# Kernel optimization log

Hardware: AMD Instinct MI355X
Metric: run time of the kernel (lower is better)

Reference implementation:

```python
import jax, jax.numpy as jnp
import numpy as np

N_NODES = 100000
N_EDGES = 1600000
N_CLASS = 26
HIDDEN = 128
K = 3  # TAGConv hops


def setup_inputs() -> dict:
    key = jax.random.key(0)
    ks = jax.random.split(key, 12)
    x = jax.random.normal(ks[0], (N_NODES, N_CLASS), dtype=jnp.float32)
    edge_index = jax.random.randint(ks[1], (2, N_EDGES), 0, N_NODES, dtype=jnp.int64)
    edge_weight = jax.random.uniform(ks[2], (N_EDGES,), dtype=jnp.float32)
    # Per-hop weights (K+1 hops incl. hop 0) for each of the 3 TAGConv layers.
    def lin(k, fan_in, fan_out):
        s = 1.0 / np.sqrt(fan_in)
        return jax.random.uniform(k, (K + 1, fan_in, fan_out), dtype=jnp.float32, minval=-s, maxval=s)
    W1 = lin(ks[3], N_CLASS, HIDDEN)
    b1 = jnp.zeros((HIDDEN,), dtype=jnp.float32)
    W2 = lin(ks[4], HIDDEN, HIDDEN)
    b2 = jnp.zeros((HIDDEN,), dtype=jnp.float32)
    W3 = lin(ks[5], HIDDEN, N_CLASS)
    b3 = jnp.zeros((N_CLASS,), dtype=jnp.float32)
    return {"x": x, "edge_index": edge_index, "edge_weight": edge_weight,
            "W1": W1, "b1": b1, "W2": W2, "b2": b2, "W3": W3, "b3": b3}


def _gcn_norm(edge_index, edge_weight, n):
    # symmetric normalization deg^-1/2 * w * deg^-1/2, no self loops (PyG TAGConv)
    row, col = edge_index[0], edge_index[1]
    deg = jax.ops.segment_sum(edge_weight, col, num_segments=n)
    dinv = jnp.where(deg > 0, jax.lax.rsqrt(jnp.maximum(deg, 1e-12)), 0.0)
    return dinv[row] * edge_weight * dinv[col]


def _tag_conv(x, row, col, norm, W, b, n):
    # out = sum_k W_k(x_k), x_0 = x, x_k = A_norm x_{k-1}
    out = x @ W[0]
    h = x
    for k in range(1, K + 1):
        h = jax.ops.segment_sum(norm[:, None] * h[row], col, num_segments=n)
        out = out + h @ W[k]
    return out + b


def reference(x, edge_index, edge_weight, W1, b1, W2, b2, W3, b3):
    n = x.shape[0]
    row, col = edge_index[0], edge_index[1]
    norm = _gcn_norm(edge_index, edge_weight, n)  # identical for all 3 layers
    h = jax.nn.elu(_tag_conv(x, row, col, norm, W1, b1, n))
    h = jax.nn.elu(_tag_conv(h, row, col, norm, W2, b2, n))
    return _tag_conv(h, row, col, norm, W3, b3, n)
```

## Files before the change

kernel.cpp:

```cpp
#include <hip/hip_runtime.h>

#define NCLS 26
#define HID 128
#define EPB 8192
#define MAXBK 512
#define BCAP 6016
typedef unsigned short ushort_t;
typedef unsigned int uint_t;
typedef unsigned long long u64;

typedef __bf16 bf16x8 __attribute__((ext_vector_type(8)));
typedef float f32x4 __attribute__((ext_vector_type(4)));
typedef unsigned int u32x4 __attribute__((ext_vector_type(4)));
typedef unsigned int u32x2 __attribute__((ext_vector_type(2)));

static __device__ __forceinline__ float b2f(ushort_t h) {
  return __uint_as_float(((uint_t)h) << 16);
}
static __device__ __forceinline__ ushort_t f2b(float f) {
  uint_t u = __float_as_uint(f);
  uint_t r = (u + 0x7fffu + ((u >> 16) & 1u)) >> 16;
  return (ushort_t)r;
}
static __device__ __forceinline__ uint_t pack2(float f0, float f1) {
  return (uint_t)f2b(f0) | ((uint_t)f2b(f1) << 16);
}
static __device__ __forceinline__ float lo16(uint_t v) { return b2f((ushort_t)(v & 0xffffu)); }
static __device__ __forceinline__ float hi16(uint_t v) { return b2f((ushort_t)(v >> 16)); }
static __device__ __forceinline__ bf16x8 ld_frag(const ushort_t* p) {
  u32x4 v = *reinterpret_cast<const u32x4*>(p);
  return __builtin_bit_cast(bf16x8, v);
}


__global__ __launch_bounds__(256) void bucket_place(
    const int* __restrict__ ei, const float* __restrict__ ew,
    int* __restrict__ gcur, u64* __restrict__ bkt, int E, int nbk) {
  __shared__ uint_t lc[MAXBK];
  __shared__ uint_t lb[MAXBK];
  int tid = threadIdx.x;
  for (int t = tid; t < nbk; t += 256) lc[t] = 0;
  __syncthreads();
  int e0 = blockIdx.x * EPB;
#pragma unroll
  for (int i = 0; i < EPB / 256; ++i) {
    int e = e0 + tid + i * 256;
    if (e < E) atomicAdd(&lc[(uint_t)ei[E + e] >> 8], 1u);
  }
  __syncthreads();
  for (int t = tid; t < nbk; t += 256) {
    uint_t c = lc[t];
    lb[t] = c ? (uint_t)t * BCAP + (uint_t)atomicAdd(&gcur[t], (int)c) : 0u;
    lc[t] = 0;
  }
  __syncthreads();
#pragma unroll
  for (int i = 0; i < EPB / 256; ++i) {
    int e = e0 + tid + i * 256;
    if (e < E) {
      uint_t r = (uint_t)ei[e];
      uint_t c = (uint_t)ei[E + e];
      uint_t b = c >> 8;
      uint_t pos = lb[b] + atomicAdd(&lc[b], 1u);
      bkt[pos] = ((u64)(r | ((c & 255u) << 24)) << 32) | (u64)__float_as_uint(ew[e]);
    }
  }
}

__global__ void scan_buckets(const int* __restrict__ gcur, int* __restrict__ mbase,
                             int nbk, int E) {
  __shared__ int s[512];
  int t = threadIdx.x;
  int v = (t < nbk) ? gcur[t] : 0;
  s[t] = v;
  __syncthreads();
  for (int off = 1; off < 512; off <<= 1) {
    int u = (t >= off) ? s[t - off] : 0;
    __syncthreads();
    s[t] += u;
    __syncthreads();
  }
  if (t < nbk) mbase[t] = s[t] - v;
  if (t == 0) mbase[nbk] = E;
}

__global__ __launch_bounds__(256) void bucket_stats(
    const u64* __restrict__ bkt, const int* __restrict__ gcur, const int* __restrict__ mbase,
    int* __restrict__ start, float* __restrict__ dinv, int n, int E) {
  int b = blockIdx.x;
  __shared__ uint_t cnt[256];
  __shared__ float deg[256];
  __shared__ int ssc[256];
  int tid = threadIdx.x;
  cnt[tid] = 0;
  deg[tid] = 0.f;
  __syncthreads();
  int fill = gcur[b];
  const u64* w = bkt + (size_t)b * BCAP;
  for (int p = tid; p < fill; p += 256) {
    u64 v = w[p];
    uint_t cl = (uint_t)(v >> 56);
    float wv = __uint_as_float((uint_t)(v & 0xffffffffULL));
    atomicAdd(&cnt[cl], 1u);
    atomicAdd(&deg[cl], wv);
  }
  __syncthreads();
  int v0 = (int)cnt[tid];
  ssc[tid] = v0;
  __syncthreads();
  for (int off = 1; off < 256; off <<= 1) {
    int u = (tid >= off) ? ssc[tid - off] : 0;
    __syncthreads();
    ssc[tid] += u;
    __syncthreads();
  }
  int node = (b << 8) + tid;
  if (node < n) {
    start[node] = mbase[b] + ssc[tid] - v0;
    float d = deg[tid];
    dinv[node] = d > 0.f ? rsqrtf(fmaxf(d, 1e-12f)) : 0.f;
  }
  if (b == 0 && tid == 0) start[n] = E;
}

__global__ __launch_bounds__(256) void bucket_emit(
    const u64* __restrict__ bkt, const int* __restrict__ gcur, const int* __restrict__ start,
    const float* __restrict__ dinv, u32x2* __restrict__ meta, int n) {
  int b = blockIdx.x;
  __shared__ uint_t lcur[256];
  int tid = threadIdx.x;
  lcur[tid] = 0;
  __syncthreads();
  int fill = gcur[b];
  const u64* w = bkt + (size_t)b * BCAP;
  for (int p = tid; p < fill; p += 256) {
    u64 v = w[p];
    uint_t hi = (uint_t)(v >> 32);
    uint_t r = hi & 0xffffffu;
    uint_t cl = hi >> 24;
    float wv = __uint_as_float((uint_t)(v & 0xffffffffULL));
    uint_t node = ((uint_t)b << 8) + cl;
    float nrm = dinv[r] * wv * dinv[node];
    uint_t slot = (uint_t)start[node] + atomicAdd(&lcur[cl], 1u);
    u32x2 m;
    m.x = r;
    m.y = __float_as_uint(nrm);
    meta[slot] = m;
  }
}

__global__ __launch_bounds__(256) void prep_misc(
    const float* __restrict__ x, uint_t* __restrict__ x32,
    const float* __restrict__ W1, ushort_t* __restrict__ Wz1,
    const float* __restrict__ W2, ushort_t* __restrict__ Wz2,
    const float* __restrict__ W3, ushort_t* __restrict__ Wz3, int n, int gconv) {
  int blk = blockIdx.x;
  int tid = threadIdx.x;
  if (blk < gconv) {
    int idx = blk * 256 + tid;
    if (idx >= n * 16) return;
    int node = idx >> 4, lane = idx & 15;
    float f0 = 0.f, f1 = 0.f;
    if (lane < 13) {
      f0 = x[node * 26 + 2 * lane];
      f1 = x[node * 26 + 2 * lane + 1];
    }
    x32[idx] = pack2(f0, f1);
  } else if (blk < gconv + 64) {
    int idx = (blk - gconv) * 256 + tid;
    int i = idx & 7, l = (idx >> 3) & 63, j = (idx >> 9) & 7, t = idx >> 12;
    int k = 8 * (l >> 4) + i;
    int col = 16 * j + (l & 15);
    float v = (k < NCLS) ? W1[((size_t)t * NCLS + k) * 128 + col] : 0.f;
    Wz1[idx] = f2b(v);
  } else if (blk < gconv + 64 + 256) {
    int idx = (blk - gconv - 64) * 256 + tid;
    int i = idx & 7, l = (idx >> 3) & 63, j = (idx >> 9) & 7, t = idx >> 12;
    int s = t >> 2, tt = t & 3;
    int k = tt * 32 + 8 * (l >> 4) + i;
    int col = 16 * j + (l & 15);
    float v = W2[((size_t)s * HID + k) * 128 + col];
    Wz2[idx] = f2b(v);
  } else {
    int idx = (blk - gconv - 64 - 256) * 256 + tid;
    int i = idx & 7, l = (idx >> 3) & 63, j = (idx >> 9) & 7, t = idx >> 12;
    int k = t * 32 + 8 * (l >> 4) + i;
    int col = 16 * j + (l & 15);
    int s = col >> 5, c = col & 31;
    float v = (c < 26) ? W3[((size_t)s * 128 + k) * 26 + c] : 0.f;
    Wz3[idx] = f2b(v);
  }
}


__global__ __launch_bounds__(256) void spmm128_bf(
    const u32x2* __restrict__ meta, const int* __restrict__ start,
    const uint_t* __restrict__ in, uint_t* __restrict__ out, int n) {
  int node = blockIdx.x * 4 + (threadIdx.x >> 6);
  int lane = threadIdx.x & 63;
  if (node >= n) return;
  int s = start[node], m = start[node + 1] - s;
  int eq = lane >> 4;
  uint_t foff = (uint_t)(lane & 15) << 4;
  const char* inb = (const char*)in;
  float a0 = 0.f, a1 = 0.f, a2 = 0.f, a3 = 0.f, a4 = 0.f, a5 = 0.f, a6 = 0.f, a7 = 0.f;
  if (m > 0) {
    const int mm = m - 1;
    u32x2 mtA0 = meta[s + (eq < m ? eq : mm)];
    u32x2 mtA1 = meta[s + (4 + eq < m ? 4 + eq : mm)];
    u32x2 mtB0 = meta[s + (8 + eq < m ? 8 + eq : mm)];
    u32x2 mtB1 = meta[s + (12 + eq < m ? 12 + eq : mm)];
    u32x4 vA0 = *reinterpret_cast<const u32x4*>(inb + (((uint_t)mtA0.x << 8) + foff));
    u32x4 vA1 = *reinterpret_cast<const u32x4*>(inb + (((uint_t)mtA1.x << 8) + foff));
    for (int base = 0; base < m; base += 8) {
      int p0 = base + 16 + eq, p1 = base + 20 + eq;
      u32x2 mtC0 = meta[s + (p0 < m ? p0 : mm)];
      u32x2 mtC1 = meta[s + (p1 < m ? p1 : mm)];
      u32x4 vB0 = *reinterpret_cast<const u32x4*>(inb + (((uint_t)mtB0.x << 8) + foff));
      u32x4 vB1 = *reinterpret_cast<const u32x4*>(inb + (((uint_t)mtB1.x << 8) + foff));
      float w0 = (base + eq < m) ? __uint_as_float(mtA0.y) : 0.f;
      float w1 = (base + 4 + eq < m) ? __uint_as_float(mtA1.y) : 0.f;
      a0 += w0 * lo16(vA0.x); a1 += w0 * hi16(vA0.x);
      a2 += w0 * lo16(vA0.y); a3 += w0 * hi16(vA0.y);
      a4 += w0 * lo16(vA0.z); a5 += w0 * hi16(vA0.z);
      a6 += w0 * lo16(vA0.w); a7 += w0 * hi16(vA0.w);
      a0 += w1 * lo16(vA1.x); a1 += w1 * hi16(vA1.x);
      a2 += w1 * lo16(vA1.y); a3 += w1 * hi16(vA1.y);
      a4 += w1 * lo16(vA1.z); a5 += w1 * hi16(vA1.z);
      a6 += w1 * lo16(vA1.w); a7 += w1 * hi16(vA1.w);
      mtA0 = mtB0; mtA1 = mtB1;
      mtB0 = mtC0; mtB1 = mtC1;
      vA0 = vB0; vA1 = vB1;
    }
  }
  a0 += __shfl_xor(a0, 16); a1 += __shfl_xor(a1, 16);
  a2 += __shfl_xor(a2, 16); a3 += __shfl_xor(a3, 16);
  a4 += __shfl_xor(a4, 16); a5 += __shfl_xor(a5, 16);
  a6 += __shfl_xor(a6, 16); a7 += __shfl_xor(a7, 16);
  a0 += __shfl_xor(a0, 32); a1 += __shfl_xor(a1, 32);
  a2 += __shfl_xor(a2, 32); a3 += __shfl_xor(a3, 32);
  a4 += __shfl_xor(a4, 32); a5 += __shfl_xor(a5, 32);
  a6 += __shfl_xor(a6, 32); a7 += __shfl_xor(a7, 32);
  if (eq == 0) {
    u32x4 o;
    o.x = pack2(a0, a1);
    o.y = pack2(a2, a3);
    o.z = pack2(a4, a5);
    o.w = pack2(a6, a7);
    *reinterpret_cast<u32x4*>(out + (size_t)node * 64 + (foff >> 2)) = o;
  }
}

__global__ __launch_bounds__(256) void spmm26_bf(
    const u32x2* __restrict__ meta, const int* __restrict__ start,
    const uint_t* __restrict__ in, const uint_t* __restrict__ add,
    uint_t* __restrict__ out, int n) {
  int node = blockIdx.x * 32 + (threadIdx.x >> 3);
  int ln = threadIdx.x & 7;
  if (node >= n) return;
  int s = start[node], m = start[node + 1] - s;
  uint_t foff = (uint_t)ln << 3;
  const char* inb = (const char*)in;
  float a0 = 0.f, a1 = 0.f, a2 = 0.f, a3 = 0.f;
  if (m > 0) {
    for (int base = 0; base < m; base += 8) {
      int j = base + ln;
      u32x2 mt = meta[s + (j < m ? j : m - 1)];
      int rr = (int)mt.x;
      float ww = (j < m) ? __uint_as_float(mt.y) : 0.f;
#pragma unroll
      for (int k = 0; k < 8; ++k) {
        uint_t r = (uint_t)__shfl(rr, k, 8);
        float wv = __shfl(ww, k, 8);
        u32x2 v = *reinterpret_cast<const u32x2*>(inb + ((r << 6) + foff));
        a0 += wv * lo16(v.x); a1 += wv * hi16(v.x);
        a2 += wv * lo16(v.y); a3 += wv * hi16(v.y);
      }
    }
  }
  if (add) {
    u32x2 v = *reinterpret_cast<const u32x2*>(add + (size_t)node * 16 + 2 * ln);
    a0 += lo16(v.x); a1 += hi16(v.x);
    a2 += lo16(v.y); a3 += hi16(v.y);
  }
  u32x2 o;
  o.x = pack2(a0, a1);
  o.y = pack2(a2, a3);
  *reinterpret_cast<u32x2*>(out + (size_t)node * 16 + 2 * ln) = o;
}

__global__ __launch_bounds__(256) void spmm26_addf(
    const u32x2* __restrict__ meta, const int* __restrict__ start,
    const uint_t* __restrict__ in, float* __restrict__ out, int n) {
  int node = blockIdx.x * 32 + (threadIdx.x >> 3);
  int ln = threadIdx.x & 7;
  if (node >= n) return;
  int s = start[node], m = start[node + 1] - s;
  uint_t foff = (uint_t)ln << 3;
  const char* inb = (const char*)in;
  float a0 = 0.f, a1 = 0.f, a2 = 0.f, a3 = 0.f;
  if (m > 0) {
    for (int base = 0; base < m; base += 8) {
      int j = base + ln;
      u32x2 mt = meta[s + (j < m ? j : m - 1)];
      int rr = (int)mt.x;
      float ww = (j < m) ? __uint_as_float(mt.y) : 0.f;
#pragma unroll
      for (int k = 0; k < 8; ++k) {
        uint_t r = (uint_t)__shfl(rr, k, 8);
        float wv = __shfl(ww, k, 8);
        u32x2 v = *reinterpret_cast<const u32x2*>(inb + ((r << 6) + foff));
        a0 += wv * lo16(v.x); a1 += wv * hi16(v.x);
        a2 += wv * lo16(v.y); a3 += wv * hi16(v.y);
      }
    }
  }
  int c0 = 4 * ln;
  if (c0 + 0 < 26) out[(size_t)node * 26 + c0 + 0] += a0;
  if (c0 + 1 < 26) out[(size_t)node * 26 + c0 + 1] += a1;
  if (c0 + 2 < 26) out[(size_t)node * 26 + c0 + 2] += a2;
  if (c0 + 3 < 26) out[(size_t)node * 26 + c0 + 3] += a3;
}

template <int KW, int NSRC, int EPI, int GROUP>
__global__ __launch_bounds__(256) void mfma_gemm(
    const ushort_t* __restrict__ A0, const ushort_t* __restrict__ A1,
    const ushort_t* __restrict__ A2, const ushort_t* __restrict__ A3,
    const ushort_t* __restrict__ Wswz, const float* __restrict__ bias,
    ushort_t* __restrict__ outb, float* __restrict__ outf, int n) {
  constexpr int KSPS = KW / 32;
  constexpr int KSTEPS = NSRC * KSPS;
  constexpr int NGROUPS = KSTEPS / GROUP;
  __shared__ ushort_t sW[GROUP * 4096];
  const int tid = threadIdx.x;
  const int w = tid >> 6;
  const int l = tid & 63;
  const int row0 = blockIdx.x * 64 + w * 16;
  const int koff = 8 * (l >> 4);
  const int arow = row0 + (l & 15);
  const int arow_c = arow < n ? arow : (n - 1);

  f32x4 acc[8];
#pragma unroll
  for (int j = 0; j < 8; ++j) acc[j] = (f32x4){0.f, 0.f, 0.f, 0.f};

  const ushort_t* const srcs[4] = {A0, A1, A2, A3};

  auto aload = [&](int t) {
    const int s = t / KSPS;
    const int tt = t - s * KSPS;
    return ld_frag(srcs[s] + (size_t)arow_c * KW + tt * 32 + koff);
  };

  bf16x8 afA[GROUP], afB[GROUP];
#pragma unroll
  for (int c = 0; c < GROUP; ++c) afA[c] = aload(c);
  u32x4 gw[2 * GROUP];
#pragma unroll
  for (int c = 0; c < GROUP; ++c) {
    const ushort_t* p = Wswz + (size_t)c * 4096 + tid * 8;
    gw[2 * c] = *reinterpret_cast<const u32x4*>(p);
    gw[2 * c + 1] = *reinterpret_cast<const u32x4*>(p + 2048);
  }

#pragma unroll
  for (int g = 0; g < NGROUPS; ++g) {
    __syncthreads();
#pragma unroll
    for (int c = 0; c < GROUP; ++c) {
      *reinterpret_cast<u32x4*>(sW + c * 4096 + tid * 8) = gw[2 * c];
      *reinterpret_cast<u32x4*>(sW + c * 4096 + tid * 8 + 2048) = gw[2 * c + 1];
    }
    if (g + 1 < NGROUPS) {
#pragma unroll
      for (int c = 0; c < GROUP; ++c) {
        const ushort_t* p = Wswz + (size_t)(g + 1) * GROUP * 4096 + (size_t)c * 4096 + tid * 8;
        gw[2 * c] = *reinterpret_cast<const u32x4*>(p);
        gw[2 * c + 1] = *reinterpret_cast<const u32x4*>(p + 2048);
      }
#pragma unroll
      for (int c = 0; c < GROUP; ++c) {
        if (g & 1)
          afA[c] = aload((g + 1) * GROUP + c);
        else
          afB[c] = aload((g + 1) * GROUP + c);
      }
    }
    __syncthreads();
#pragma unroll
    for (int tg = 0; tg < GROUP; ++tg) {
      bf16x8 af = (g & 1) ? afB[tg] : afA[tg];
      const ushort_t* wp = sW + tg * 4096 + l * 8;
#pragma unroll
      for (int j = 0; j < 8; ++j) {
        bf16x8 bfr = ld_frag(wp + j * 64 * 8);
        acc[j] = __builtin_amdgcn_mfma_f32_16x16x32_bf16(af, bfr, acc[j], 0, 0, 0);
      }
    }
  }

  const int ccol = l & 15;
  const int crow0 = row0 + 4 * (l >> 4);
#pragma unroll
  for (int j = 0; j < 8; ++j) {
    if (EPI == 0) {
      int col = 16 * j + ccol;
      float bi = bias[col];
#pragma unroll
      for (int r = 0; r < 4; ++r) {
        int row = crow0 + r;
        if (row >= n) continue;
        float v = acc[j][r] + bi;
        v = v > 0.f ? v : (__expf(v) - 1.f);
        outb[(size_t)row * 128 + col] = f2b(v);
      }
    } else {
      int slot = j >> 1;
      int c = 16 * (j & 1) + ccol;
#pragma unroll
      for (int r = 0; r < 4; ++r) {
        int row = crow0 + r;
        if (row >= n) continue;
        float v = acc[j][r];
        if (slot == 0) {
          if (c < 26) outf[(size_t)row * 26 + c] = v + bias[c];
        } else {
          outb[((size_t)(slot - 1) * n + row) * 32 + c] = f2b(v);
        }
      }
    }
  }
}


extern "C" void kernel_launch(void* const* d_in, const int* in_sizes, int n_in,
                              void* d_out, int out_size, void* d_ws, size_t ws_size,
                              hipStream_t stream) {
  const float* x  = (const float*)d_in[0];
  const int*   ei = (const int*)d_in[1];
  const float* ew = (const float*)d_in[2];
  const float* W1 = (const float*)d_in[3];
  const float* b1 = (const float*)d_in[4];
  const float* W2 = (const float*)d_in[5];
  const float* b2 = (const float*)d_in[6];
  const float* W3 = (const float*)d_in[7];
  const float* b3 = (const float*)d_in[8];
  float* out = (float*)d_out;

  const int n = in_sizes[0] / NCLS;
  const int E = in_sizes[2];
  const int nbk = (n + 255) >> 8;

  char* w = (char*)d_ws;
  auto alloc = [&](size_t bytes) {
    char* p = w;
    w += (bytes + 255) / 256 * 256;
    return p;
  };
  uint_t* H0 = (uint_t*)alloc((size_t)n * 64 * 4);
  uint_t* P1 = (uint_t*)alloc((size_t)n * 64 * 4);
  uint_t* P2 = (uint_t*)alloc((size_t)n * 64 * 4);
  uint_t* P3 = (uint_t*)alloc((size_t)n * 64 * 4);
  uint_t* H1 = (uint_t*)alloc((size_t)n * 64 * 4);
  uint_t* x32 = (uint_t*)alloc((size_t)n * 16 * 4);
  uint_t* q1  = (uint_t*)alloc((size_t)n * 16 * 4);
  uint_t* q2  = (uint_t*)alloc((size_t)n * 16 * 4);
  uint_t* q3  = (uint_t*)alloc((size_t)n * 16 * 4);
  uint_t* zb  = (uint_t*)alloc((size_t)n * 48 * 4);
  ushort_t* Wz1 = (ushort_t*)alloc(4 * 4096 * 2);
  ushort_t* Wz2 = (ushort_t*)alloc(16 * 4096 * 2);
  ushort_t* Wz3 = (ushort_t*)alloc(4 * 4096 * 2);
  u64*   bkt  = (u64*)zb;
  u32x2* meta = (u32x2*)alloc((size_t)E * 8);
  int*   start = (int*)alloc((size_t)(n + 1) * 4);
  float* dinv  = (float*)alloc((size_t)n * 4);
  int*   gcur  = (int*)alloc(MAXBK * 4);
  int*   mbase = (int*)alloc((MAXBK + 1) * 4);

  const int ab = (E + EPB - 1) / EPB;
  const int gconv = (n * 16 + 255) / 256;

  prep_misc<<<gconv + 64 + 256 + 64, 256, 0, stream>>>(x, x32, W1, Wz1, W2, Wz2, W3, Wz3,
                                                       n, gconv);

  hipMemsetAsync(gcur, 0, MAXBK * 4, stream);
  bucket_place<<<ab, 256, 0, stream>>>(ei, ew, gcur, bkt, E, nbk);
  scan_buckets<<<1, 512, 0, stream>>>(gcur, mbase, nbk, E);
  bucket_stats<<<nbk, 256, 0, stream>>>(bkt, gcur, mbase, start, dinv, n, E);
  bucket_emit<<<nbk, 256, 0, stream>>>(bkt, gcur, start, dinv, meta, n);

  const int g128 = (n + 3) / 4;
  const int g26  = (n + 31) / 32;
  const int gg   = (n + 63) / 64;

  spmm26_bf<<<g26, 256, 0, stream>>>(meta, start, x32, nullptr, q1, n);
  spmm26_bf<<<g26, 256, 0, stream>>>(meta, start, q1, nullptr, q2, n);
  spmm26_bf<<<g26, 256, 0, stream>>>(meta, start, q2, nullptr, q3, n);
  mfma_gemm<32, 4, 0, 4><<<gg, 256, 0, stream>>>(
      (const ushort_t*)x32, (const ushort_t*)q1, (const ushort_t*)q2, (const ushort_t*)q3,
      Wz1, b1, (ushort_t*)H0, nullptr, n);

  spmm128_bf<<<g128, 256, 0, stream>>>(meta, start, H0, P1, n);
  spmm128_bf<<<g128, 256, 0, stream>>>(meta, start, P1, P2, n);
  spmm128_bf<<<g128, 256, 0, stream>>>(meta, start, P2, P3, n);
  mfma_gemm<128, 4, 0, 4><<<gg, 256, 0, stream>>>(
      (const ushort_t*)H0, (const ushort_t*)P1, (const ushort_t*)P2, (const ushort_t*)P3,
      Wz2, b2, (ushort_t*)H1, nullptr, n);

  mfma_gemm<128, 1, 1, 4><<<gg, 256, 0, stream>>>(
      (const ushort_t*)H1, (const ushort_t*)H1, (const ushort_t*)H1, (const ushort_t*)H1,
      Wz3, b3, (ushort_t*)zb, out, n);

  uint_t* z1 = zb;
  uint_t* z2 = zb + (size_t)n * 16;
  uint_t* z3 = zb + (size_t)n * 32;
  spmm26_bf<<<g26, 256, 0, stream>>>(meta, start, z3, z2, q1, n);
  spmm26_bf<<<g26, 256, 0, stream>>>(meta, start, q1, z1, q2, n);
  spmm26_addf<<<g26, 256, 0, stream>>>(meta, start, q2, out, n);
}
```

Baseline: 452.6 us.

## Pad per-node CSR edge lists to multiples of eight with zero entries

Measured after the change: 455.5 us. No clear change (+0.6%).

```diff
diff --git a/kernel.cpp b/kernel.cpp
--- a/kernel.cpp
+++ b/kernel.cpp
@@ -67,26 +67,9 @@
   }
 }
 
-__global__ void scan_buckets(const int* __restrict__ gcur, int* __restrict__ mbase,
-                             int nbk, int E) {
-  __shared__ int s[512];
-  int t = threadIdx.x;
-  int v = (t < nbk) ? gcur[t] : 0;
-  s[t] = v;
-  __syncthreads();
-  for (int off = 1; off < 512; off <<= 1) {
-    int u = (t >= off) ? s[t - off] : 0;
-    __syncthreads();
-    s[t] += u;
-    __syncthreads();
-  }
-  if (t < nbk) mbase[t] = s[t] - v;
-  if (t == 0) mbase[nbk] = E;
-}
-
 __global__ __launch_bounds__(256) void bucket_stats(
-    const u64* __restrict__ bkt, const int* __restrict__ gcur, const int* __restrict__ mbase,
-    int* __restrict__ start, float* __restrict__ dinv, int n, int E) {
+    const u64* __restrict__ bkt, const int* __restrict__ gcur,
+    int* __restrict__ start, int* __restrict__ pbs, float* __restrict__ dinv, int n) {
   int b = blockIdx.x;
   __shared__ uint_t cnt[256];
   __shared__ float deg[256];
@@ -105,8 +88,8 @@
     atomicAdd(&deg[cl], wv);
   }
   __syncthreads();
-  int v0 = (int)cnt[tid];
-  ssc[tid] = v0;
+  int pc = ((int)cnt[tid] + 7) & ~7;
+  ssc[tid] = pc;
   __syncthreads();
   for (int off = 1; off < 256; off <<= 1) {
     int u = (tid >= off) ? ssc[tid - off] : 0;
@@ -116,19 +99,47 @@
   }
   int node = (b << 8) + tid;
   if (node < n) {
-    start[node] = mbase[b] + ssc[tid] - v0;
+    start[node] = ssc[tid] - pc;
     float d = deg[tid];
     dinv[node] = d > 0.f ? rsqrtf(fmaxf(d, 1e-12f)) : 0.f;
   }
-  if (b == 0 && tid == 0) start[n] = E;
+  if (tid == 255) pbs[b] = ssc[255];
+}
+
+__global__ void scan_pb(const int* __restrict__ pbs, int* __restrict__ pbase,
+                        int* __restrict__ start, int nbk, int n) {
+  __shared__ int s[512];
+  int t = threadIdx.x;
+  int v = (t < nbk) ? pbs[t] : 0;
+  s[t] = v;
+  __syncthreads();
+  for (int off = 1; off < 512; off <<= 1) {
+    int u = (t >= off) ? s[t - off] : 0;
+    __syncthreads();
+    s[t] += u;
+    __syncthreads();
+  }
+  if (t < nbk) pbase[t] = s[t] - v;
+  if (t == 0) {
+    pbase[nbk] = s[nbk - 1 < 512 ? nbk - 1 : 511];
+    start[n] = pbase[nbk];
+  }
 }
 
 __global__ __launch_bounds__(256) void bucket_emit(
-    const u64* __restrict__ bkt, const int* __restrict__ gcur, const int* __restrict__ start,
-    const float* __restrict__ dinv, u32x2* __restrict__ meta, int n) {
+    const u64* __restrict__ bkt, const int* __restrict__ gcur, const int* __restrict__ pbase,
+    int* __restrict__ start, const float* __restrict__ dinv, u32x2* __restrict__ meta, int n) {
   int b = blockIdx.x;
   __shared__ uint_t lcur[256];
+  __shared__ int sstart[256];
   int tid = threadIdx.x;
+  int node = (b << 8) + tid;
+  int bb = pbase[b];
+  int fin = 0;
+  if (node < n) {
+    fin = start[node] + bb;
+    sstart[tid] = fin;
+  }
   lcur[tid] = 0;
   __syncthreads();
   int fill = gcur[b];
@@ -139,13 +150,23 @@
     uint_t r = hi & 0xffffffu;
     uint_t cl = hi >> 24;
     float wv = __uint_as_float((uint_t)(v & 0xffffffffULL));
-    uint_t node = ((uint_t)b << 8) + cl;
-    float nrm = dinv[r] * wv * dinv[node];
-    uint_t slot = (uint_t)start[node] + atomicAdd(&lcur[cl], 1u);
+    uint_t nd = ((uint_t)b << 8) + cl;
+    float nrm = dinv[r] * wv * dinv[nd];
+    uint_t slot = (uint_t)sstart[cl] + atomicAdd(&lcur[cl], 1u);
     u32x2 m;
     m.x = r;
     m.y = __float_as_uint(nrm);
     meta[slot] = m;
+  }
+  __syncthreads();
+  if (node < n) {
+    start[node] = fin;
+    int c = (int)lcur[tid];
+    int pc = (c + 7) & ~7;
+    u32x2 z;
+    z.x = 0u;
+    z.y = 0u;
+    for (int i = c; i < pc; ++i) meta[fin + i] = z;
   }
 }
 
@@ -199,27 +220,33 @@
   int node = blockIdx.x * 4 + (threadIdx.x >> 6);
   int lane = threadIdx.x & 63;
   if (node >= n) return;
-  int s = start[node], m = start[node + 1] - s;
+  int s = start[node], mp = start[node + 1] - s;
   int eq = lane >> 4;
   uint_t foff = (uint_t)(lane & 15) << 4;
   const char* inb = (const char*)in;
   float a0 = 0.f, a1 = 0.f, a2 = 0.f, a3 = 0.f, a4 = 0.f, a5 = 0.f, a6 = 0.f, a7 = 0.f;
-  if (m > 0) {
-    const int mm = m - 1;
-    u32x2 mtA0 = meta[s + (eq < m ? eq : mm)];
-    u32x2 mtA1 = meta[s + (4 + eq < m ? 4 + eq : mm)];
-    u32x2 mtB0 = meta[s + (8 + eq < m ? 8 + eq : mm)];
-    u32x2 mtB1 = meta[s + (12 + eq < m ? 12 + eq : mm)];
+  if (mp > 0) {
+    u32x2 mtA0 = meta[s + eq];
+    u32x2 mtA1 = meta[s + 4 + eq];
+    int i8 = 8 + eq;
+    if (i8 >= mp) i8 = mp - 1;
+    int i12 = 12 + eq;
+    if (i12 >= mp) i12 = mp - 1;
+    u32x2 mtB0 = meta[s + i8];
+    u32x2 mtB1 = meta[s + i12];
     u32x4 vA0 = *reinterpret_cast<const u32x4*>(inb + (((uint_t)mtA0.x << 8) + foff));
     u32x4 vA1 = *reinterpret_cast<const u32x4*>(inb + (((uint_t)mtA1.x << 8) + foff));
-    for (int base = 0; base < m; base += 8) {
-      int p0 = base + 16 + eq, p1 = base + 20 + eq;
-      u32x2 mtC0 = meta[s + (p0 < m ? p0 : mm)];
-      u32x2 mtC1 = meta[s + (p1 < m ? p1 : mm)];
+    for (int base = 0; base < mp; base += 8) {
+      int p0 = base + 16 + eq;
+      p0 = p0 < mp ? p0 : mp - 1;
+      int p1 = base + 20 + eq;
+      p1 = p1 < mp ? p1 : mp - 1;
+      u32x2 mtC0 = meta[s + p0];
+      u32x2 mtC1 = meta[s + p1];
       u32x4 vB0 = *reinterpret_cast<const u32x4*>(inb + (((uint_t)mtB0.x << 8) + foff));
       u32x4 vB1 = *reinterpret_cast<const u32x4*>(inb + (((uint_t)mtB1.x << 8) + foff));
-      float w0 = (base + eq < m) ? __uint_as_float(mtA0.y) : 0.f;
-      float w1 = (base + 4 + eq < m) ? __uint_as_float(mtA1.y) : 0.f;
+      float w0 = __uint_as_float(mtA0.y);
+      float w1 = __uint_as_float(mtA1.y);
       a0 += w0 * lo16(vA0.x); a1 += w0 * hi16(vA0.x);
       a2 += w0 * lo16(vA0.y); a3 += w0 * hi16(vA0.y);
       a4 += w0 * lo16(vA0.z); a5 += w0 * hi16(vA0.z);
@@ -258,24 +285,21 @@
   int node = blockIdx.x * 32 + (threadIdx.x >> 3);
   int ln = threadIdx.x & 7;
   if (node >= n) return;
-  int s = start[node], m = start[node + 1] - s;
+  int s = start[node], mp = start[node + 1] - s;
   uint_t foff = (uint_t)ln << 3;
   const char* inb = (const char*)in;
   float a0 = 0.f, a1 = 0.f, a2 = 0.f, a3 = 0.f;
-  if (m > 0) {
-    for (int base = 0; base < m; base += 8) {
-      int j = base + ln;
-      u32x2 mt = meta[s + (j < m ? j : m - 1)];
-      int rr = (int)mt.x;
-      float ww = (j < m) ? __uint_as_float(mt.y) : 0.f;
-#pragma unroll
-      for (int k = 0; k < 8; ++k) {
-        uint_t r = (uint_t)__shfl(rr, k, 8);
-        float wv = __shfl(ww, k, 8);
-        u32x2 v = *reinterpret_cast<const u32x2*>(inb + ((r << 6) + foff));
-        a0 += wv * lo16(v.x); a1 += wv * hi16(v.x);
-        a2 += wv * lo16(v.y); a3 += wv * hi16(v.y);
-      }
+  for (int base = 0; base < mp; base += 8) {
+    u32x2 mt = meta[s + base + ln];
+    int rr = (int)mt.x;
+    float ww = __uint_as_float(mt.y);
+#pragma unroll
+    for (int k = 0; k < 8; ++k) {
+      uint_t r = (uint_t)__shfl(rr, k, 8);
+      float wv = __shfl(ww, k, 8);
+      u32x2 v = *reinterpret_cast<const u32x2*>(inb + ((r << 6) + foff));
+      a0 += wv * lo16(v.x); a1 += wv * hi16(v.x);
+      a2 += wv * lo16(v.y); a3 += wv * hi16(v.y);
     }
   }
   if (add) {
@@ -295,24 +319,21 @@
   int node = blockIdx.x * 32 + (threadIdx.x >> 3);
   int ln = threadIdx.x & 7;
   if (node >= n) return;
-  int s = start[node], m = start[node + 1] - s;
+  int s = start[node], mp = start[node + 1] - s;
   uint_t foff = (uint_t)ln << 3;
   const char* inb = (const char*)in;
   float a0 = 0.f, a1 = 0.f, a2 = 0.f, a3 = 0.f;
-  if (m > 0) {
-    for (int base = 0; base < m; base += 8) {
-      int j = base + ln;
-      u32x2 mt = meta[s + (j < m ? j : m - 1)];
-      int rr = (int)mt.x;
-      float ww = (j < m) ? __uint_as_float(mt.y) : 0.f;
-#pragma unroll
-      for (int k = 0; k < 8; ++k) {
-        uint_t r = (uint_t)__shfl(rr, k, 8);
-        float wv = __shfl(ww, k, 8);
-        u32x2 v = *reinterpret_cast<const u32x2*>(inb + ((r << 6) + foff));
-        a0 += wv * lo16(v.x); a1 += wv * hi16(v.x);
-        a2 += wv * lo16(v.y); a3 += wv * hi16(v.y);
-      }
+  for (int base = 0; base < mp; base += 8) {
+    u32x2 mt = meta[s + base + ln];
+    int rr = (int)mt.x;
+    float ww = __uint_as_float(mt.y);
+#pragma unroll
+    for (int k = 0; k < 8; ++k) {
+      uint_t r = (uint_t)__shfl(rr, k, 8);
+      float wv = __shfl(ww, k, 8);
+      u32x2 v = *reinterpret_cast<const u32x2*>(inb + ((r << 6) + foff));
+      a0 += wv * lo16(v.x); a1 += wv * hi16(v.x);
+      a2 += wv * lo16(v.y); a3 += wv * hi16(v.y);
     }
   }
   int c0 = 4 * ln;
@@ -471,11 +492,12 @@
   ushort_t* Wz2 = (ushort_t*)alloc(16 * 4096 * 2);
   ushort_t* Wz3 = (ushort_t*)alloc(4 * 4096 * 2);
   u64*   bkt  = (u64*)zb;
-  u32x2* meta = (u32x2*)alloc((size_t)E * 8);
+  u32x2* meta = (u32x2*)alloc(((size_t)E + 7 * (size_t)n + 64) * 8);
   int*   start = (int*)alloc((size_t)(n + 1) * 4);
   float* dinv  = (float*)alloc((size_t)n * 4);
   int*   gcur  = (int*)alloc(MAXBK * 4);
-  int*   mbase = (int*)alloc((MAXBK + 1) * 4);
+  int*   pbs   = (int*)alloc(MAXBK * 4);
+  int*   pbase = (int*)alloc((MAXBK + 1) * 4);
 
   const int ab = (E + EPB - 1) / EPB;
   const int gconv = (n * 16 + 255) / 256;
@@ -485,9 +507,9 @@
 
   hipMemsetAsync(gcur, 0, MAXBK * 4, stream);
   bucket_place<<<ab, 256, 0, stream>>>(ei, ew, gcur, bkt, E, nbk);
-  scan_buckets<<<1, 512, 0, stream>>>(gcur, mbase, nbk, E);
-  bucket_stats<<<nbk, 256, 0, stream>>>(bkt, gcur, mbase, start, dinv, n, E);
-  bucket_emit<<<nbk, 256, 0, stream>>>(bkt, gcur, start, dinv, meta, n);
+  bucket_stats<<<nbk, 256, 0, stream>>>(bkt, gcur, start, pbs, dinv, n);
+  scan_pb<<<1, 512, 0, stream>>>(pbs, pbase, start, nbk, n);
+  bucket_emit<<<nbk, 256, 0, stream>>>(bkt, gcur, pbase, start, dinv, meta, n);
 
   const int g128 = (n + 3) / 4;
   const int g26  = (n + 31) / 32;
```
